# Kernel tuning notes

Measured on AMD Instinct MI355X. Metric: run time of the kernel, lower is better.

## Reference

```python
import jax, jax.numpy as jnp
import numpy as np

BS, SL, NC = 1024, 512, 50


def setup_inputs() -> dict:
    key = jax.random.key(0)
    k1, k2, k3, k4 = jax.random.split(key, 4)
    inputs = jax.random.normal(k1, (BS, SL, NC), dtype=jnp.float32)
    # variable sentence lengths; mask is True on PAD positions (as in torch code)
    lengths = jax.random.randint(k2, (BS,), SL // 4, SL + 1)
    masks = jnp.arange(SL)[None, :] >= lengths[:, None]
    tag_indices = jax.random.randint(k3, (BS, SL), 0, NC)
    transitions = jax.random.normal(k4, (NC, NC), dtype=jnp.float32) * 0.1
    return {"inputs": inputs, "transitions": transitions,
            "masks": masks, "tag_indices": tag_indices}


def _crf_loss(inputs, transitions, masks, tag_indices):
    bs, sl, nc = inputs.shape
    # unary score: emission of the gold tag at each valid position
    unary = jnp.take_along_axis(inputs, tag_indices[..., None], axis=2)[..., 0]  # [bs,sl]
    unary = jnp.where(masks, 0.0, unary).sum(axis=1)
    # binary score: transition gold[t] -> gold[t+1] where t+1 valid
    binary = transitions[tag_indices[:, :-1], tag_indices[:, 1:]]  # [bs,sl-1]
    binary = jnp.where(masks[:, 1:], 0.0, binary).sum(axis=1)
    # log partition via forward algorithm (fused scan over time)
    alphas0 = inputs[:, 0, :]  # [bs,nc]
    rest_x = jnp.swapaxes(inputs[:, 1:, :], 0, 1)  # [sl-1,bs,nc]
    rest_m = jnp.swapaxes(masks[:, 1:], 0, 1)      # [sl-1,bs]

    def step(alphas, xm):
        x, m = xm
        scores = alphas[:, :, None] + transitions[None, :, :]  # [bs,nc_from,nc_to]
        new_alphas = x + jax.scipy.special.logsumexp(scores, axis=1)
        # carry alphas unchanged at padded positions (masked_scatter_ in torch)
        alphas = jnp.where(m[:, None], alphas, new_alphas)
        return alphas, None

    alphas, _ = jax.lax.scan(step, alphas0, (rest_x, rest_m))
    log_norm = jax.scipy.special.logsumexp(alphas, axis=1)  # [bs]
    log_likelihood = unary + binary - log_norm
    loss = -log_likelihood.sum() / bs  # batch_average=True
    return loss


def reference(inputs, transitions, masks, tag_indices):
    loss = _crf_loss(inputs, transitions, masks, tag_indices)
    return loss, transitions
```

## Files before the change

kernel.cpp:

```cpp
#include <hip/hip_runtime.h>


#define BS 1024
#define SL 512
#define NC 50

__global__ void pre_kernel(const float* __restrict__ trans, float* __restrict__ out) {
  const int k = blockIdx.x * 256 + threadIdx.x;
  if (k == 0) out[0] = 0.0f;
  if (k < NC * NC) out[1 + k] = trans[k];
}

__launch_bounds__(128)
__global__ void crf_scan(const float* __restrict__ inputs,
                         const float* __restrict__ trans,
                         const int* __restrict__ masks,
                         const int* __restrict__ tags,
                         float* __restrict__ out) {
  __shared__ float T_s[NC * NC];
  __shared__ __align__(16) float bc[2][64];
  __shared__ float Bb_s[64];
  __shared__ float scal[2];

  const int tid = threadIdx.x;
  const int w = tid >> 6;
  const int j = tid & 63;
  const int b = blockIdx.x;
  const bool jv = (j < NC);
  const int jj = jv ? j : (NC - 1);

  for (int k = tid; k < NC * NC; k += 128) T_s[k] = trans[k];
  __syncthreads();

  const float* __restrict__ xr = inputs + (size_t)b * SL * NC;
  const int* __restrict__ mr = masks + b * SL;
  const int* __restrict__ gr = tags + b * SL;

  int L = SL;
  for (int c = 0; c < 8; ++c) {
    const int m = mr[c * 64 + j];
    const unsigned long long bal = __ballot(m != 0);
    if (bal) { L = c * 64 + (int)__builtin_ctzll(bal); break; }
  }
  const int mid = L >> 1;

  float A;
  float Cf = 0.0f;

  if (w == 0) {
    float eTc[NC];
#pragma unroll
    for (int i = 0; i < NC; ++i) eTc[i] = __expf(T_s[i * NC + jj]);

    A = __expf(xr[jj]);

    float xc = xr[1 * NC + jj];
    float pa = xr[2 * NC + jj];
    float pb = xr[3 * NC + jj];
    float pc = xr[4 * NC + jj];

    for (int t = 1; t <= mid; ++t) {
      const float ex = __expf(xc);
      bc[0][j] = A;
      float s0 = 0.f, s1 = 0.f, s2 = 0.f, s3 = 0.f;
#pragma unroll
      for (int i = 0; i < 12; ++i) {
        const float4 e = *reinterpret_cast<const float4*>(&bc[0][i * 4]);
        s0 = fmaf(e.x, eTc[i * 4 + 0], s0);
        s1 = fmaf(e.y, eTc[i * 4 + 1], s1);
        s2 = fmaf(e.z, eTc[i * 4 + 2], s2);
        s3 = fmaf(e.w, eTc[i * 4 + 3], s3);
      }
      {
        const float2 e = *reinterpret_cast<const float2*>(&bc[0][48]);
        s0 = fmaf(e.x, eTc[48], s0);
        s1 = fmaf(e.y, eTc[49], s1);
      }
      const float s = (s0 + s1) + (s2 + s3);
      const float Ap = ex * s;
      const float r =
          __int_as_float(__builtin_amdgcn_readfirstlane(__float_as_int(Ap)));
      Cf += __logf(r);
      A = Ap * __builtin_amdgcn_rcpf(r);

      xc = pa; pa = pb; pb = pc;
      int tn = t + 4; tn = (tn < SL) ? tn : (SL - 1);
      pc = xr[tn * NC + jj];
    }
  } else {
    float eTr[NC];
#pragma unroll
    for (int i = 0; i < NC; ++i) eTr[i] = __expf(T_s[jj * NC + i]);

    float u = 0.0f;
    for (int c = 0; c < 8; ++c) {
      const int t = c * 64 + j;
      const int tg = gr[t];
      const bool valid = (t < L);
      const float xv = xr[t * NC + tg];
      if (valid) u += xv;
      if (valid && t >= 1) u += T_s[gr[t - 1] * NC + tg];
    }
#pragma unroll
    for (int m = 32; m; m >>= 1) u += __shfl_xor(u, m, 64);

    float B = 1.0f;
    float Cb = 0.0f;
    float xc = xr[(L - 1) * NC + jj];
    float pa = xr[(L - 2) * NC + jj];
    float pb = xr[(L - 3) * NC + jj];
    float pc = xr[(L - 4) * NC + jj];

    for (int t = L - 1; t > mid; --t) {
      const float ex = __expf(xc);
      bc[1][j] = ex * B;
      float s0 = 0.f, s1 = 0.f, s2 = 0.f, s3 = 0.f;
#pragma unroll
      for (int i = 0; i < 12; ++i) {
        const float4 e = *reinterpret_cast<const float4*>(&bc[1][i * 4]);
        s0 = fmaf(e.x, eTr[i * 4 + 0], s0);
        s1 = fmaf(e.y, eTr[i * 4 + 1], s1);
        s2 = fmaf(e.z, eTr[i * 4 + 2], s2);
        s3 = fmaf(e.w, eTr[i * 4 + 3], s3);
      }
      {
        const float2 e = *reinterpret_cast<const float2*>(&bc[1][48]);
        s0 = fmaf(e.x, eTr[48], s0);
        s1 = fmaf(e.y, eTr[49], s1);
      }
      const float s = (s0 + s1) + (s2 + s3);
      const float r =
          __int_as_float(__builtin_amdgcn_readfirstlane(__float_as_int(s)));
      Cb += __logf(r);
      B = s * __builtin_amdgcn_rcpf(r);

      xc = pa; pa = pb; pb = pc;
      int tn = t - 4; tn = (tn >= 0) ? tn : 0;
      pc = xr[tn * NC + jj];
    }

    Bb_s[j] = B;
    if (j == 0) { scal[0] = Cb; scal[1] = u; }
  }

  __syncthreads();

  if (w == 0) {
    float prod = jv ? (A * Bb_s[j]) : 0.0f;
#pragma unroll
    for (int m = 32; m; m >>= 1) prod += __shfl_xor(prod, m, 64);
    if (j == 0) {
      const float logZ = Cf + scal[0] + __logf(prod);
      const float ll = scal[1] - logZ;
      atomicAdd(out, -ll * (1.0f / (float)BS));
    }
  }
}

extern "C" void kernel_launch(void* const* d_in, const int* in_sizes, int n_in,
                              void* d_out, int out_size, void* d_ws, size_t ws_size,
                              hipStream_t stream) {
  const float* inputs = (const float*)d_in[0];
  const float* trans  = (const float*)d_in[1];
  const int*   masks  = (const int*)d_in[2];
  const int*   tags   = (const int*)d_in[3];
  float* out = (float*)d_out;

  pre_kernel<<<(NC * NC + 256) / 256, 256, 0, stream>>>(trans, out);
  crf_scan<<<BS, 128, 0, stream>>>(inputs, trans, masks, tags, out);
}
```

Before: 277.9 us.

## Broadcast CRF recurrence state via readlane and fuse the init kernel

Each step of the forward and backward recurrences used to publish its state through shared memory and read it back with vector loads. It now pulls the 50 lane values straight into scalars with readlane, so no LDS round trip sits on the serial dependency chain. The per-step normalization is taken from the previous state, which moves the readfirstlane off the critical path. The unary and binary gold-path scores are now split across both waves, and the separate pre-kernel is folded into block 0. The mask length is now counted with popcount. Output zeroing was dropped, so the atomicAdd relies on the output buffer already being zero.

```diff
diff --git a/kernel.cpp b/kernel.cpp
--- a/kernel.cpp
+++ b/kernel.cpp
@@ -5,20 +5,16 @@
 #define SL 512
 #define NC 50
 
-__global__ void pre_kernel(const float* __restrict__ trans, float* __restrict__ out) {
-  const int k = blockIdx.x * 256 + threadIdx.x;
-  if (k == 0) out[0] = 0.0f;
-  if (k < NC * NC) out[1 + k] = trans[k];
-}
+#define RLF(v, i) __int_as_float(__builtin_amdgcn_readlane(__float_as_int(v), i))
+#define RFLF(v)   __int_as_float(__builtin_amdgcn_readfirstlane(__float_as_int(v)))
 
 __launch_bounds__(128)
-__global__ void crf_scan(const float* __restrict__ inputs,
-                         const float* __restrict__ trans,
-                         const int* __restrict__ masks,
-                         const int* __restrict__ tags,
-                         float* __restrict__ out) {
+__global__ void crf_fused(const float* __restrict__ inputs,
+                          const float* __restrict__ trans,
+                          const int* __restrict__ masks,
+                          const int* __restrict__ tags,
+                          float* __restrict__ out) {
   __shared__ float T_s[NC * NC];
-  __shared__ __align__(16) float bc[2][64];
   __shared__ float Bb_s[64];
   __shared__ float scal[2];
 
@@ -32,128 +28,125 @@
   for (int k = tid; k < NC * NC; k += 128) T_s[k] = trans[k];
   __syncthreads();
 
+  if (b == 0) {
+    for (int k = tid; k < NC * NC; k += 128) out[1 + k] = T_s[k];
+  }
+
   const float* __restrict__ xr = inputs + (size_t)b * SL * NC;
   const int* __restrict__ mr = masks + b * SL;
   const int* __restrict__ gr = tags + b * SL;
 
-  int L = SL;
+  int nm = 0;
+#pragma unroll
   for (int c = 0; c < 8; ++c) {
-    const int m = mr[c * 64 + j];
-    const unsigned long long bal = __ballot(m != 0);
-    if (bal) { L = c * 64 + (int)__builtin_ctzll(bal); break; }
+    nm += (int)__popcll(__ballot(mr[c * 64 + j] != 0));
   }
+  const int L = SL - nm;
   const int mid = L >> 1;
 
-  float A;
-  float Cf = 0.0f;
+  float u = 0.0f;
+#pragma unroll
+  for (int c = 0; c < 4; ++c) {
+    const int t = (w * 4 + c) * 64 + j;
+    const int g = gr[t];
+    const int tp = (t >= 1) ? t - 1 : 0;
+    const int gp = gr[tp];
+    float add = xr[(size_t)t * NC + g];
+    if (t >= 1) add += T_s[gp * NC + g];
+    if (t < L) u += add;
+  }
+#pragma unroll
+  for (int m = 32; m; m >>= 1) u += __shfl_xor(u, m, 64);
 
   if (w == 0) {
     float eTc[NC];
 #pragma unroll
     for (int i = 0; i < NC; ++i) eTc[i] = __expf(T_s[i * NC + jj]);
 
-    A = __expf(xr[jj]);
+    float Au = __expf(xr[jj]);
+    float C = 0.0f;
 
     float xc = xr[1 * NC + jj];
-    float pa = xr[2 * NC + jj];
-    float pb = xr[3 * NC + jj];
-    float pc = xr[4 * NC + jj];
+    float p1 = xr[2 * NC + jj];
+    float p2 = xr[3 * NC + jj];
+    float p3 = xr[4 * NC + jj];
 
     for (int t = 1; t <= mid; ++t) {
       const float ex = __expf(xc);
-      bc[0][j] = A;
-      float s0 = 0.f, s1 = 0.f, s2 = 0.f, s3 = 0.f;
+      const float r = RFLF(Au);
+      float s0 = RLF(Au, 0) * eTc[0];
+      float s1 = RLF(Au, 1) * eTc[1];
+      float s2 = RLF(Au, 2) * eTc[2];
+      float s3 = RLF(Au, 3) * eTc[3];
 #pragma unroll
-      for (int i = 0; i < 12; ++i) {
-        const float4 e = *reinterpret_cast<const float4*>(&bc[0][i * 4]);
-        s0 = fmaf(e.x, eTc[i * 4 + 0], s0);
-        s1 = fmaf(e.y, eTc[i * 4 + 1], s1);
-        s2 = fmaf(e.z, eTc[i * 4 + 2], s2);
-        s3 = fmaf(e.w, eTc[i * 4 + 3], s3);
+      for (int i = 4; i < 48; i += 4) {
+        s0 = fmaf(RLF(Au, i + 0), eTc[i + 0], s0);
+        s1 = fmaf(RLF(Au, i + 1), eTc[i + 1], s1);
+        s2 = fmaf(RLF(Au, i + 2), eTc[i + 2], s2);
+        s3 = fmaf(RLF(Au, i + 3), eTc[i + 3], s3);
       }
-      {
-        const float2 e = *reinterpret_cast<const float2*>(&bc[0][48]);
-        s0 = fmaf(e.x, eTc[48], s0);
-        s1 = fmaf(e.y, eTc[49], s1);
-      }
-      const float s = (s0 + s1) + (s2 + s3);
-      const float Ap = ex * s;
-      const float r =
-          __int_as_float(__builtin_amdgcn_readfirstlane(__float_as_int(Ap)));
-      Cf += __logf(r);
-      A = Ap * __builtin_amdgcn_rcpf(r);
+      s0 = fmaf(RLF(Au, 48), eTc[48], s0);
+      s1 = fmaf(RLF(Au, 49), eTc[49], s1);
+      const float dot = (s0 + s1) + (s2 + s3);
+      C += __logf(r);
+      Au = (ex * __builtin_amdgcn_rcpf(r)) * dot;
+      xc = p1; p1 = p2; p2 = p3;
+      p3 = xr[(t + 4) * NC + jj];
+    }
+    const float rf = RFLF(Au);
+    C += __logf(rf);
+    const float A = Au * __builtin_amdgcn_rcpf(rf);
 
-      xc = pa; pa = pb; pb = pc;
-      int tn = t + 4; tn = (tn < SL) ? tn : (SL - 1);
-      pc = xr[tn * NC + jj];
+    __syncthreads();
+    float prod = jv ? (A * Bb_s[j]) : 0.0f;
+#pragma unroll
+    for (int m = 32; m; m >>= 1) prod += __shfl_xor(prod, m, 64);
+    if (j == 0) {
+      const float logZ = C + scal[0] + __logf(prod);
+      const float ll = (u + scal[1]) - logZ;
+      atomicAdd(out, -ll * (1.0f / (float)BS));
     }
   } else {
     float eTr[NC];
 #pragma unroll
     for (int i = 0; i < NC; ++i) eTr[i] = __expf(T_s[jj * NC + i]);
 
-    float u = 0.0f;
-    for (int c = 0; c < 8; ++c) {
-      const int t = c * 64 + j;
-      const int tg = gr[t];
-      const bool valid = (t < L);
-      const float xv = xr[t * NC + tg];
-      if (valid) u += xv;
-      if (valid && t >= 1) u += T_s[gr[t - 1] * NC + tg];
-    }
-#pragma unroll
-    for (int m = 32; m; m >>= 1) u += __shfl_xor(u, m, 64);
+    float Bu = 1.0f;
+    float Cb = 0.0f;
 
-    float B = 1.0f;
-    float Cb = 0.0f;
     float xc = xr[(L - 1) * NC + jj];
-    float pa = xr[(L - 2) * NC + jj];
-    float pb = xr[(L - 3) * NC + jj];
-    float pc = xr[(L - 4) * NC + jj];
+    float p1 = xr[(L - 2) * NC + jj];
+    float p2 = xr[(L - 3) * NC + jj];
+    float p3 = xr[(L - 4) * NC + jj];
 
     for (int t = L - 1; t > mid; --t) {
       const float ex = __expf(xc);
-      bc[1][j] = ex * B;
-      float s0 = 0.f, s1 = 0.f, s2 = 0.f, s3 = 0.f;
+      const float r = RFLF(Bu);
+      const float V = ex * Bu;
+      float s0 = RLF(V, 0) * eTr[0];
+      float s1 = RLF(V, 1) * eTr[1];
+      float s2 = RLF(V, 2) * eTr[2];
+      float s3 = RLF(V, 3) * eTr[3];
 #pragma unroll
-      for (int i = 0; i < 12; ++i) {
-        const float4 e = *reinterpret_cast<const float4*>(&bc[1][i * 4]);
-        s0 = fmaf(e.x, eTr[i * 4 + 0], s0);
-        s1 = fmaf(e.y, eTr[i * 4 + 1], s1);
-        s2 = fmaf(e.z, eTr[i * 4 + 2], s2);
-        s3 = fmaf(e.w, eTr[i * 4 + 3], s3);
+      for (int i = 4; i < 48; i += 4) {
+        s0 = fmaf(RLF(V, i + 0), eTr[i + 0], s0);
+        s1 = fmaf(RLF(V, i + 1), eTr[i + 1], s1);
+        s2 = fmaf(RLF(V, i + 2), eTr[i + 2], s2);
+        s3 = fmaf(RLF(V, i + 3), eTr[i + 3], s3);
       }
-      {
-        const float2 e = *reinterpret_cast<const float2*>(&bc[1][48]);
-        s0 = fmaf(e.x, eTr[48], s0);
-        s1 = fmaf(e.y, eTr[49], s1);
-      }
-      const float s = (s0 + s1) + (s2 + s3);
-      const float r =
-          __int_as_float(__builtin_amdgcn_readfirstlane(__float_as_int(s)));
+      s0 = fmaf(RLF(V, 48), eTr[48], s0);
+      s1 = fmaf(RLF(V, 49), eTr[49], s1);
+      const float dot = (s0 + s1) + (s2 + s3);
       Cb += __logf(r);
-      B = s * __builtin_amdgcn_rcpf(r);
-
-      xc = pa; pa = pb; pb = pc;
-      int tn = t - 4; tn = (tn >= 0) ? tn : 0;
-      pc = xr[tn * NC + jj];
+      Bu = __builtin_amdgcn_rcpf(r) * dot;
+      xc = p1; p1 = p2; p2 = p3;
+      p3 = xr[(t - 4) * NC + jj];
     }
-
-    Bb_s[j] = B;
+    const float rf = RFLF(Bu);
+    Cb += __logf(rf);
+    Bb_s[j] = Bu * __builtin_amdgcn_rcpf(rf);
     if (j == 0) { scal[0] = Cb; scal[1] = u; }
-  }
-
-  __syncthreads();
-
-  if (w == 0) {
-    float prod = jv ? (A * Bb_s[j]) : 0.0f;
-#pragma unroll
-    for (int m = 32; m; m >>= 1) prod += __shfl_xor(prod, m, 64);
-    if (j == 0) {
-      const float logZ = Cf + scal[0] + __logf(prod);
-      const float ll = scal[1] - logZ;
-      atomicAdd(out, -ll * (1.0f / (float)BS));
-    }
+    __syncthreads();
   }
 }
 
@@ -166,6 +159,5 @@
   const int*   tags   = (const int*)d_in[3];
   float* out = (float*)d_out;
 
-  pre_kernel<<<(NC * NC + 256) / 256, 256, 0, stream>>>(trans, out);
-  crf_scan<<<BS, 128, 0, stream>>>(inputs, trans, masks, tags, out);
+  crf_fused<<<BS, 128, 0, stream>>>(inputs, trans, masks, tags, out);
 }
```

Result: slower. 311.8 us (+12.2%).
